# Optimization experiments

Hardware: AMD Instinct MI355X
Metric: run time of the kernel (lower is better)

The kernel has to match this reference:

```python
import jax, jax.numpy as jnp
import numpy as np

H, W = 512, 512
B, C = 16, 3
PCT = 3.0  # normalization_percentile_threshold


def _make_filter_map(h, w, d0_ratio=0.05, bn=1):
    d0 = int(max(d0_ratio * min(h, w) // 2, 1))  # = 12 for 512x512
    i = np.arange(h, dtype=np.float64)[:, None]
    j = np.arange(w, dtype=np.float64)[None, :]
    d = np.full((h, w), np.inf)
    for cx, cy in ((0, 0), (0, w - 1), (h - 1, w - 1), (h - 1, 0)):
        d = np.minimum(d, np.sqrt((i - cx) ** 2 + (j - cy) ** 2))
    fm = 1.0 / (1.0 + (d0 / (d + 1.0)) ** (2 * bn))
    # torch code assigns filter_map[j, i] -> transpose (no-op for square sizes)
    return jnp.asarray(fm.T.astype(np.float32))


def setup_inputs() -> dict:
    key = jax.random.key(0)
    k1, k2 = jax.random.split(key)
    x = jax.random.normal(k1, (B, C, H, W), dtype=jnp.float32)
    mask = (jax.random.uniform(k2, (B, C, H, W)) > 0.2).astype(jnp.float32)
    filter_map = _make_filter_map(H, W)
    return {"x": x, "mask": mask, "filter_map": filter_map}


def reference(x, mask, filter_map):
    b, c, h, w = x.shape
    n = h * w
    # median_padding: torch.median returns the lower middle element -> sorted index (n-1)//2
    med = jnp.sort(x.reshape(b, c, n), axis=-1)[..., (n - 1) // 2] + 0.2  # (B,C)
    xp = mask * x + (1.0 - mask) * med[:, :, None, None]
    # Butterworth high-pass in Fourier domain
    hfc = jnp.abs(jnp.fft.ifft2(jnp.fft.fft2(xp) * filter_map)).astype(jnp.float32)
    # per-(n,c) percentile normalization; .int() truncates toward zero -> jnp.trunc
    temp = jnp.trunc(hfc * 256.0) / 256.0
    lo = jnp.percentile(temp, PCT, axis=(-2, -1), keepdims=True)
    hi = jnp.percentile(temp, 100.0 - PCT, axis=(-2, -1), keepdims=True)
    res = (hfc - lo) / (hi - lo)
    return res * mask
```

## Files before the change

### kernel.cpp

```cpp
#include <hip/hip_runtime.h>
#include <math.h>


#define HN 512
#define WN 512
#define NPIX (HN * WN)
#define NCH 48
#define MED_K 131071u
#define TWOPI 6.283185307179586f

typedef unsigned int u32;
typedef float f4v __attribute__((ext_vector_type(4)));

__device__ __constant__ u32 PRANKS[4] = {7864u, 7865u, 254278u, 254279u};

__device__ __forceinline__ int rev8_9(int i) { return ((i & 7) << 6) | (i & 56) | (i >> 6); }

__device__ __forceinline__ int swz(int e) { return e ^ ((e >> 4) & 0xF); }

#define WB() __builtin_amdgcn_wave_barrier()

__device__ __forceinline__ u32 f2key(float f) {
  u32 u = __float_as_uint(f);
  return u ^ ((u & 0x80000000u) ? 0xFFFFFFFFu : 0x80000000u);
}
__device__ __forceinline__ float key2f(u32 k) {
  u32 u = (k & 0x80000000u) ? (k ^ 0x80000000u) : ~k;
  return __uint_as_float(u);
}

__device__ __forceinline__ float2 cadd(float2 a, float2 b) { return make_float2(a.x + b.x, a.y + b.y); }
__device__ __forceinline__ float2 csub(float2 a, float2 b) { return make_float2(a.x - b.x, a.y - b.y); }
__device__ __forceinline__ float2 cmul(float2 a, float2 b) {
  return make_float2(a.x * b.x - a.y * b.y, a.x * b.y + a.y * b.x);
}

template <bool INV>
__device__ __forceinline__ void dft8(float2* r) {
  const float S2 = 0.70710678118654752f;
  float2 e0, e1, e2, e3, o0, o1, o2, o3;
  {
    float2 t0 = cadd(r[0], r[4]), t1 = csub(r[0], r[4]);
    float2 t2 = cadd(r[2], r[6]), t3 = csub(r[2], r[6]);
    e0 = cadd(t0, t2); e2 = csub(t0, t2);
    if (!INV) { e1 = make_float2(t1.x + t3.y, t1.y - t3.x); e3 = make_float2(t1.x - t3.y, t1.y + t3.x); }
    else      { e1 = make_float2(t1.x - t3.y, t1.y + t3.x); e3 = make_float2(t1.x + t3.y, t1.y - t3.x); }
  }
  {
    float2 t0 = cadd(r[1], r[5]), t1 = csub(r[1], r[5]);
    float2 t2 = cadd(r[3], r[7]), t3 = csub(r[3], r[7]);
    o0 = cadd(t0, t2); o2 = csub(t0, t2);
    if (!INV) { o1 = make_float2(t1.x + t3.y, t1.y - t3.x); o3 = make_float2(t1.x - t3.y, t1.y + t3.x); }
    else      { o1 = make_float2(t1.x - t3.y, t1.y + t3.x); o3 = make_float2(t1.x + t3.y, t1.y - t3.x); }
  }
  float2 w1o, w2o, w3o;
  if (!INV) {
    w1o = make_float2(S2 * (o1.x + o1.y), S2 * (o1.y - o1.x));
    w2o = make_float2(o2.y, -o2.x);
    w3o = make_float2(S2 * (o3.y - o3.x), -S2 * (o3.x + o3.y));
  } else {
    w1o = make_float2(S2 * (o1.x - o1.y), S2 * (o1.x + o1.y));
    w2o = make_float2(-o2.y, o2.x);
    w3o = make_float2(-S2 * (o3.x + o3.y), S2 * (o3.x - o3.y));
  }
  r[0] = cadd(e0, o0); r[4] = csub(e0, o0);
  r[1] = cadd(e1, w1o); r[5] = csub(e1, w1o);
  r[2] = cadd(e2, w2o); r[6] = csub(e2, w2o);
  r[3] = cadd(e3, w3o); r[7] = csub(e3, w3o);
}

__device__ __forceinline__ void twid(float2* r, float ang) {
  float sn, cs;
  __sincosf(ang, &sn, &cs);
  float2 w = make_float2(cs, sn);
  float2 wj = w;
  r[1] = cmul(r[1], wj);
  #pragma unroll
  for (int j = 2; j < 8; ++j) { wj = cmul(wj, w); r[j] = cmul(r[j], wj); }
}

__device__ void scan_find(const u32* __restrict__ h, int per, u32 rank,
                          u32* out_bin, u32* out_pref) {
  __shared__ u32 csum[256], cpre[256];
  int t = threadIdx.x;
  u32 s = 0;
  for (int i = 0; i < per; ++i) s += h[t * per + i];
  csum[t] = s;
  __syncthreads();
  if (t == 0) { u32 a = 0; for (int i = 0; i < 256; ++i) { cpre[i] = a; a += csum[i]; } }
  __syncthreads();
  if (cpre[t] <= rank && rank < cpre[t] + csum[t]) {
    u32 acc = cpre[t];
    for (int i = 0; i < per; ++i) {
      u32 c = h[t * per + i];
      if (rank < acc + c) { *out_bin = (u32)(t * per + i); *out_pref = acc; break; }
      acc += c;
    }
  }
  __syncthreads();
}


__global__ __launch_bounds__(256) void kmed1(const float4* __restrict__ x4, u32* __restrict__ h1) {
  int ch = blockIdx.x >> 4, s = blockIdx.x & 15;
  __shared__ u32 lh[4096];
  for (int i = threadIdx.x; i < 4096; i += 256) lh[i] = 0;
  __syncthreads();
  const float4* p = x4 + (size_t)ch * (NPIX / 4) + (size_t)s * (NPIX / 64);
  for (int i = threadIdx.x; i < NPIX / 64; i += 256) {
    float4 v = p[i];
    atomicAdd(&lh[f2key(v.x) >> 20], 1u);
    atomicAdd(&lh[f2key(v.y) >> 20], 1u);
    atomicAdd(&lh[f2key(v.z) >> 20], 1u);
    atomicAdd(&lh[f2key(v.w) >> 20], 1u);
  }
  __syncthreads();
  u32* h = h1 + (size_t)ch * 4096;
  for (int i = threadIdx.x; i < 4096; i += 256) { u32 c = lh[i]; if (c) atomicAdd(&h[i], c); }
}

__global__ __launch_bounds__(256) void kscan1(const u32* __restrict__ h1, u32* sel1, u32* pref1) {
  __shared__ u32 b, p;
  scan_find(h1 + (size_t)blockIdx.x * 4096, 16, MED_K, &b, &p);
  if (threadIdx.x == 0) { sel1[blockIdx.x] = b; pref1[blockIdx.x] = p; }
}

__global__ __launch_bounds__(256) void kmed2(const float4* __restrict__ x4, u32* __restrict__ h2,
                                             const u32* __restrict__ sel1) {
  int ch = blockIdx.x >> 4, s = blockIdx.x & 15;
  u32 sh = sel1[ch];
  __shared__ u32 lh[4096];
  for (int i = threadIdx.x; i < 4096; i += 256) lh[i] = 0;
  __syncthreads();
  const float4* p = x4 + (size_t)ch * (NPIX / 4) + (size_t)s * (NPIX / 64);
  for (int i = threadIdx.x; i < NPIX / 64; i += 256) {
    float4 v = p[i];
    u32 k;
    k = f2key(v.x); if ((k >> 20) == sh) atomicAdd(&lh[(k >> 8) & 0xFFFu], 1u);
    k = f2key(v.y); if ((k >> 20) == sh) atomicAdd(&lh[(k >> 8) & 0xFFFu], 1u);
    k = f2key(v.z); if ((k >> 20) == sh) atomicAdd(&lh[(k >> 8) & 0xFFFu], 1u);
    k = f2key(v.w); if ((k >> 20) == sh) atomicAdd(&lh[(k >> 8) & 0xFFFu], 1u);
  }
  __syncthreads();
  u32* h = h2 + (size_t)ch * 4096;
  for (int i = threadIdx.x; i < 4096; i += 256) { u32 c = lh[i]; if (c) atomicAdd(&h[i], c); }
}

__global__ __launch_bounds__(256) void kscan2(const u32* __restrict__ h2, const u32* __restrict__ pref1,
                                              u32* sel2, u32* pref2) {
  __shared__ u32 b, p;
  scan_find(h2 + (size_t)blockIdx.x * 4096, 16, MED_K - pref1[blockIdx.x], &b, &p);
  if (threadIdx.x == 0) { sel2[blockIdx.x] = b; pref2[blockIdx.x] = p; }
}

__global__ __launch_bounds__(256) void kmed3(const float4* __restrict__ x4, u32* __restrict__ h3,
                                             const u32* __restrict__ sel1, const u32* __restrict__ sel2) {
  int ch = blockIdx.x >> 4, s = blockIdx.x & 15;
  u32 pre = (sel1[ch] << 12) | sel2[ch];
  __shared__ u32 lh[256];
  lh[threadIdx.x] = 0;
  __syncthreads();
  const float4* p = x4 + (size_t)ch * (NPIX / 4) + (size_t)s * (NPIX / 64);
  for (int i = threadIdx.x; i < NPIX / 64; i += 256) {
    float4 v = p[i];
    u32 k;
    k = f2key(v.x); if ((k >> 8) == pre) atomicAdd(&lh[k & 0xFFu], 1u);
    k = f2key(v.y); if ((k >> 8) == pre) atomicAdd(&lh[k & 0xFFu], 1u);
    k = f2key(v.z); if ((k >> 8) == pre) atomicAdd(&lh[k & 0xFFu], 1u);
    k = f2key(v.w); if ((k >> 8) == pre) atomicAdd(&lh[k & 0xFFu], 1u);
  }
  __syncthreads();
  u32 c = lh[threadIdx.x];
  if (c) atomicAdd(&h3[(size_t)ch * 256 + threadIdx.x], c);
}

__global__ __launch_bounds__(256) void kscan3(const u32* __restrict__ h3, const u32* __restrict__ sel1,
                                              const u32* __restrict__ sel2, const u32* __restrict__ pref1,
                                              const u32* __restrict__ pref2, float* med) {
  int ch = blockIdx.x;
  __shared__ u32 b, p;
  scan_find(h3 + (size_t)ch * 256, 1, MED_K - pref1[ch] - pref2[ch], &b, &p);
  if (threadIdx.x == 0) {
    u32 key = (sel1[ch] << 20) | (sel2[ch] << 8) | b;
    med[ch] = key2f(key) + 0.2f;
  }
}


__global__ __launch_bounds__(256) void kperm(const float* __restrict__ fmap, float* __restrict__ fmp) {
  int c = blockIdx.x;
  for (int e = threadIdx.x; e < HN; e += 256)
    fmp[(size_t)c * HN + e] = fmap[(size_t)rev8_9(e) * WN + rev8_9(c)] * (1.0f / (float)NPIX);
}


__global__ __launch_bounds__(256) void krow_fwd(const float* __restrict__ x, const float* __restrict__ mask,
                                                const float* __restrict__ med, float2* __restrict__ cbuf, int ch0) {
  int lch = blockIdx.x >> 7, rb = blockIdx.x & 127;
  int gch = ch0 + lch;
  int lane = threadIdx.x & 63, r = threadIdx.x >> 6;
  int row = rb * 4 + r;
  __shared__ float2 lds[4][512];
  float2* L = lds[r];
  float mv = med[gch];
  const float* xr = x + (size_t)gch * NPIX + (size_t)row * WN;
  const float* mr = mask + (size_t)gch * NPIX + (size_t)row * WN;
  float2 rg[8];
  #pragma unroll
  for (int m = 0; m < 8; ++m) {
    float xv = xr[lane + 64 * m], mm = mr[lane + 64 * m];
    rg[m] = make_float2(mm * xv + (1.0f - mm) * mv, 0.0f);
  }
  dft8<false>(rg);
  twid(rg, (float)lane * (-TWOPI / 512.0f));
  #pragma unroll
  for (int j = 0; j < 8; ++j) L[swz(lane + 64 * j)] = rg[j];
  WB();
  int eb = 64 * (lane >> 3) + (lane & 7);
  #pragma unroll
  for (int m = 0; m < 8; ++m) rg[m] = L[swz(eb + 8 * m)];
  dft8<false>(rg);
  twid(rg, (float)(lane & 7) * (-TWOPI / 64.0f));
  #pragma unroll
  for (int j = 0; j < 8; ++j) L[swz(eb + 8 * j)] = rg[j];
  WB();
  int pcb = (8 * lane) ^ ((lane >> 1) & 0xF);
  #pragma unroll
  for (int m = 0; m < 8; ++m) rg[m] = L[pcb ^ m];
  dft8<false>(rg);
  #pragma unroll
  for (int j = 0; j < 8; ++j) L[pcb ^ j] = rg[j];
  WB();
  float2* cb = cbuf + (size_t)lch * NPIX + (size_t)row * WN;
  #pragma unroll
  for (int q = 0; q < 4; ++q) {
    int e = 2 * (lane + 64 * q);
    int s = swz(e);
    float2 a = L[s], b = L[s ^ 1];
    *(float4*)(cb + e) = make_float4(a.x, a.y, b.x, b.y);
  }
}


__global__ __launch_bounds__(1024, 8) void kcol(float2* __restrict__ cbuf, const float* __restrict__ fmp) {
  int lch = blockIdx.x >> 5;
  int c0 = (blockIdx.x & 31) << 4;
  int tid = threadIdx.x;
  int lane = tid & 63, w = tid >> 6;
  __shared__ float2 lds[16][512];
  float2* L = lds[w];
  size_t base = (size_t)lch * NPIX + c0;
  #pragma unroll
  for (int it = 0; it < 4; ++it) {
    int g = it * 1024 + tid;
    int h = g >> 3, qq = g & 7;
    float4 v = *(const float4*)(cbuf + base + (size_t)h * WN + 2 * qq);
    int sh = swz(h);
    lds[2 * qq][sh]     = make_float2(v.x, v.y);
    lds[2 * qq + 1][sh] = make_float2(v.z, v.w);
  }
  __syncthreads();
  float2 rg[8];
  int eb = 64 * (lane >> 3) + (lane & 7);
  int pcb = (8 * lane) ^ ((lane >> 1) & 0xF);
  #pragma unroll
  for (int m = 0; m < 8; ++m) rg[m] = L[swz(lane + 64 * m)];
  dft8<false>(rg);
  twid(rg, (float)lane * (-TWOPI / 512.0f));
  #pragma unroll
  for (int j = 0; j < 8; ++j) L[swz(lane + 64 * j)] = rg[j];
  WB();
  #pragma unroll
  for (int m = 0; m < 8; ++m) rg[m] = L[swz(eb + 8 * m)];
  dft8<false>(rg);
  twid(rg, (float)(lane & 7) * (-TWOPI / 64.0f));
  #pragma unroll
  for (int j = 0; j < 8; ++j) L[swz(eb + 8 * j)] = rg[j];
  WB();
  #pragma unroll
  for (int m = 0; m < 8; ++m) rg[m] = L[pcb ^ m];
  dft8<false>(rg);
  {
    const float* fp = fmp + (size_t)(c0 + w) * HN + 8 * lane;
    float4 f0 = *(const float4*)fp, f1 = *(const float4*)(fp + 4);
    rg[0].x *= f0.x; rg[0].y *= f0.x;  rg[1].x *= f0.y; rg[1].y *= f0.y;
    rg[2].x *= f0.z; rg[2].y *= f0.z;  rg[3].x *= f0.w; rg[3].y *= f0.w;
    rg[4].x *= f1.x; rg[4].y *= f1.x;  rg[5].x *= f1.y; rg[5].y *= f1.y;
    rg[6].x *= f1.z; rg[6].y *= f1.z;  rg[7].x *= f1.w; rg[7].y *= f1.w;
  }
  dft8<true>(rg);
  #pragma unroll
  for (int j = 0; j < 8; ++j) L[pcb ^ j] = rg[j];
  WB();
  #pragma unroll
  for (int m = 0; m < 8; ++m) rg[m] = L[swz(eb + 8 * m)];
  twid(rg, (float)(lane & 7) * (TWOPI / 64.0f));
  dft8<true>(rg);
  #pragma unroll
  for (int j = 0; j < 8; ++j) L[swz(eb + 8 * j)] = rg[j];
  WB();
  #pragma unroll
  for (int m = 0; m < 8; ++m) rg[m] = L[swz(lane + 64 * m)];
  twid(rg, (float)lane * (TWOPI / 512.0f));
  dft8<true>(rg);
  #pragma unroll
  for (int j = 0; j < 8; ++j) L[swz(lane + 64 * j)] = rg[j];
  __syncthreads();
  #pragma unroll
  for (int it = 0; it < 4; ++it) {
    int g = it * 1024 + tid;
    int h = g >> 3, qq = g & 7;
    int sh = swz(h);
    float2 a = lds[2 * qq][sh], b = lds[2 * qq + 1][sh];
    *(float4*)(cbuf + base + (size_t)h * WN + 2 * qq) = make_float4(a.x, a.y, b.x, b.y);
  }
}


__global__ __launch_bounds__(256) void krow_inv(const float2* __restrict__ cbuf, float* __restrict__ out,
                                                u32* __restrict__ hc, int ch0) {
  int lch = blockIdx.x >> 7, rb = blockIdx.x & 127;
  int gch = ch0 + lch;
  int lane = threadIdx.x & 63, r = threadIdx.x >> 6;
  int row = rb * 4 + r;
  __shared__ float2 lds[4][512];
  __shared__ u32 lh[4][256];
  float2* L = lds[r];
  u32* H = lh[r];
  #pragma unroll
  for (int i = 0; i < 4; ++i) H[lane + 64 * i] = 0;
  const float2* cb = cbuf + (size_t)lch * NPIX + (size_t)row * WN;
  #pragma unroll
  for (int q = 0; q < 4; ++q) {
    int e = 2 * (lane + 64 * q);
    float4 v = *(const float4*)(cb + e);
    int s = swz(e);
    L[s]     = make_float2(v.x, v.y);
    L[s ^ 1] = make_float2(v.z, v.w);
  }
  WB();
  float2 rg[8];
  int pcb = (8 * lane) ^ ((lane >> 1) & 0xF);
  #pragma unroll
  for (int m = 0; m < 8; ++m) rg[m] = L[pcb ^ m];
  dft8<true>(rg);
  #pragma unroll
  for (int j = 0; j < 8; ++j) L[pcb ^ j] = rg[j];
  WB();
  int eb = 64 * (lane >> 3) + (lane & 7);
  #pragma unroll
  for (int m = 0; m < 8; ++m) rg[m] = L[swz(eb + 8 * m)];
  twid(rg, (float)(lane & 7) * (TWOPI / 64.0f));
  dft8<true>(rg);
  #pragma unroll
  for (int j = 0; j < 8; ++j) L[swz(eb + 8 * j)] = rg[j];
  WB();
  #pragma unroll
  for (int m = 0; m < 8; ++m) rg[m] = L[swz(lane + 64 * m)];
  twid(rg, (float)lane * (TWOPI / 512.0f));
  dft8<true>(rg);
  float* orow = out + (size_t)gch * NPIX + (size_t)row * WN;
  u32 binv[8];
  #pragma unroll
  for (int j = 0; j < 8; ++j) {
    float mg = sqrtf(rg[j].x * rg[j].x + rg[j].y * rg[j].y);
    orow[lane + 64 * j] = mg;
    binv[j] = ((u32)fminf(mg * 256.0f, 65535.0f)) >> 8;
  }
  #pragma unroll 1
  for (int j = 0; j < 8; ++j) {
    u32 bin = binv[j];
    unsigned long long todo = __ballot(1);
    while (todo) {
      int src = (int)(__ffsll((unsigned long long)todo) - 1);
      u32 b = (u32)__shfl((int)bin, src);
      unsigned long long mt = __ballot(bin == b);
      if (lane == src) atomicAdd(&H[b], (u32)__popcll(mt));
      todo &= ~mt;
    }
  }
  #pragma unroll
  for (int i = 0; i < 4; ++i) {
    u32 c = H[lane + 64 * i];
    if (c) atomicAdd(&hc[(size_t)gch * 256 + lane + 64 * i], c);
  }
}


__global__ __launch_bounds__(256) void kpcts1(const u32* __restrict__ hc, u32* selc, u32* prefc) {
  int ch = blockIdx.x;
  __shared__ u32 b, p;
  for (int q = 0; q < 4; ++q) {
    scan_find(hc + (size_t)ch * 256, 1, PRANKS[q], &b, &p);
    if (threadIdx.x == 0) { selc[ch * 4 + q] = b; prefc[ch * 4 + q] = p; }
    __syncthreads();
  }
}

__global__ __launch_bounds__(256) void kpctf(const float4* __restrict__ out4, u32* __restrict__ hf,
                                             const u32* __restrict__ selc) {
  int ch = blockIdx.x >> 3, s = blockIdx.x & 7;
  u32 t0 = selc[ch * 4 + 0], t1 = selc[ch * 4 + 1], t2 = selc[ch * 4 + 2], t3 = selc[ch * 4 + 3];
  __shared__ u32 lh[1024];
  for (int i = threadIdx.x; i < 1024; i += 256) lh[i] = 0;
  __syncthreads();
  const float4* p = out4 + (size_t)ch * (NPIX / 4) + (size_t)s * (NPIX / 32);
  for (int i = threadIdx.x; i < NPIX / 32; i += 256) {
    float4 v = p[i];
    float vv[4] = {v.x, v.y, v.z, v.w};
    #pragma unroll
    for (int j = 0; j < 4; ++j) {
      u32 bin = (u32)fminf(vv[j] * 256.0f, 65535.0f);
      u32 cb = bin >> 8, fb = bin & 255u;
      if (cb == t0) atomicAdd(&lh[0 * 256 + fb], 1u);
      if (cb == t1) atomicAdd(&lh[1 * 256 + fb], 1u);
      if (cb == t2) atomicAdd(&lh[2 * 256 + fb], 1u);
      if (cb == t3) atomicAdd(&lh[3 * 256 + fb], 1u);
    }
  }
  __syncthreads();
  for (int i = threadIdx.x; i < 1024; i += 256) {
    u32 c = lh[i];
    if (c) atomicAdd(&hf[(size_t)ch * 1024 + i], c);
  }
}

__global__ __launch_bounds__(256) void kpcts2(const u32* __restrict__ hf, const u32* __restrict__ selc,
                                              const u32* __restrict__ prefc, float* lov, float* invv) {
  int ch = blockIdx.x;
  __shared__ u32 b, p;
  __shared__ u32 bins[4];
  for (int q = 0; q < 4; ++q) {
    scan_find(hf + (size_t)ch * 1024 + q * 256, 1, PRANKS[q] - prefc[ch * 4 + q], &b, &p);
    if (threadIdx.x == 0) bins[q] = (selc[ch * 4 + q] << 8) | b;
    __syncthreads();
  }
  if (threadIdx.x == 0) {
    double vlo = 0.03 * (double)(NPIX - 1);
    double vhi = 0.97 * (double)(NPIX - 1);
    double glo = vlo - floor(vlo);
    double ghi = vhi - floor(vhi);
    double l0 = bins[0] / 256.0, l1 = bins[1] / 256.0;
    double h0 = bins[2] / 256.0, h1 = bins[3] / 256.0;
    double lo = l0 + glo * (l1 - l0);
    double hi = h0 + ghi * (h1 - h0);
    lov[ch] = (float)lo;
    invv[ch] = (float)(1.0 / (hi - lo));
  }
}


__global__ __launch_bounds__(256) void kfinal(float4* __restrict__ o4, const float4* __restrict__ m4,
                                              const float* __restrict__ lov, const float* __restrict__ invv) {
  size_t i = (size_t)blockIdx.x * 256 + threadIdx.x;
  int ch = (int)(i >> 16);
  float lo = lov[ch], iv = invv[ch];
  float4 o = o4[i], m = m4[i];
  f4v res;
  res.x = (o.x - lo) * iv * m.x;
  res.y = (o.y - lo) * iv * m.y;
  res.z = (o.z - lo) * iv * m.z;
  res.w = (o.w - lo) * iv * m.w;
  __builtin_nontemporal_store(res, (f4v*)&o4[i]);
}


extern "C" void kernel_launch(void* const* d_in, const int* in_sizes, int n_in,
                              void* d_out, int out_size, void* d_ws, size_t ws_size,
                              hipStream_t stream) {
  (void)in_sizes; (void)n_in; (void)out_size;
  const float* x = (const float*)d_in[0];
  const float* mask = (const float*)d_in[1];
  const float* fmap = (const float*)d_in[2];
  float* out = (float*)d_out;
  char* ws = (char*)d_ws;

  size_t off = 0;
  u32* h1 = (u32*)(ws + off); off += (size_t)NCH * 4096 * 4;
  u32* h2 = (u32*)(ws + off); off += (size_t)NCH * 4096 * 4;
  u32* h3 = (u32*)(ws + off); off += (size_t)NCH * 256 * 4;
  u32* hc = (u32*)(ws + off); off += (size_t)NCH * 256 * 4;
  u32* hf = (u32*)(ws + off); off += (size_t)NCH * 1024 * 4;
  const size_t HIST_BYTES = off;
  u32* sel1  = (u32*)(ws + off); off += NCH * 4;
  u32* pref1 = (u32*)(ws + off); off += NCH * 4;
  u32* sel2  = (u32*)(ws + off); off += NCH * 4;
  u32* pref2 = (u32*)(ws + off); off += NCH * 4;
  u32* selc  = (u32*)(ws + off); off += NCH * 16;
  u32* prefc = (u32*)(ws + off); off += NCH * 16;
  float* med  = (float*)(ws + off); off += NCH * 4;
  float* lov  = (float*)(ws + off); off += NCH * 4;
  float* invv = (float*)(ws + off); off += NCH * 4;
  off = (off + 4095) & ~(size_t)4095;
  float* fmp = (float*)(ws + off); off += (size_t)NPIX * 4;
  off = (off + 255) & ~(size_t)255;
  float2* cbuf = (float2*)(ws + off);

  size_t avail = (ws_size > off) ? ws_size - off : 0;
  int cpc = 1;
  const int cands[8] = {48, 24, 16, 12, 8, 4, 2, 1};
  for (int i = 0; i < 8; ++i) {
    if ((size_t)cands[i] * NPIX * sizeof(float2) <= avail) { cpc = cands[i]; break; }
  }

  (void)hipMemsetAsync(ws, 0, HIST_BYTES, stream);
  kperm<<<WN, 256, 0, stream>>>(fmap, fmp);

  kmed1<<<NCH * 16, 256, 0, stream>>>((const float4*)x, h1);
  kscan1<<<NCH, 256, 0, stream>>>(h1, sel1, pref1);
  kmed2<<<NCH * 16, 256, 0, stream>>>((const float4*)x, h2, sel1);
  kscan2<<<NCH, 256, 0, stream>>>(h2, pref1, sel2, pref2);
  kmed3<<<NCH * 16, 256, 0, stream>>>((const float4*)x, h3, sel1, sel2);
  kscan3<<<NCH, 256, 0, stream>>>(h3, sel1, sel2, pref1, pref2, med);

  for (int ch0 = 0; ch0 < NCH; ch0 += cpc) {
    int cc = (NCH - ch0 < cpc) ? (NCH - ch0) : cpc;
    krow_fwd<<<cc * 128, 256, 0, stream>>>(x, mask, med, cbuf, ch0);
    kcol<<<cc * 32, 1024, 0, stream>>>(cbuf, fmp);
    krow_inv<<<cc * 128, 256, 0, stream>>>(cbuf, out, hc, ch0);
  }

  kpcts1<<<NCH, 256, 0, stream>>>(hc, selc, prefc);
  kpctf<<<NCH * 8, 256, 0, stream>>>((const float4*)out, hf, selc);
  kpcts2<<<NCH, 256, 0, stream>>>(hf, selc, prefc, lov, invv);

  kfinal<<<(NCH * NPIX / 4) / 256, 256, 0, stream>>>((float4*)out, (const float4*)mask, lov, invv);
}
```

Measured before the change: 366.8 us.

## Compact median candidates and build percentile histogram inside inverse row FFT

The three-pass radix median is replaced by one histogram pass plus a pass that compacts the keys falling in the median's top-level bin into a candidate list. A single block per channel then resolves the remaining bits from that list, avoiding a third full read of x. The percentile stage now builds a 4096-bin histogram (1/256 resolution) directly in krow_inv, which removes the coarse/fine two-pass histogram that reread the whole output. It also splits kmed1's shared histogram in two to reduce atomic contention and caps the FFT channel chunk at 16. The costs are heavier shared-memory atomics and LDS use in krow_inv, and a fixed candidate capacity that would break correctness if more than 32768 keys land in the median's bin.

Measured after the change: 379.9 us. +3.6%, slower.

```diff
diff --git a/kernel.cpp b/kernel.cpp
--- a/kernel.cpp
+++ b/kernel.cpp
@@ -8,6 +8,7 @@
 #define NCH 48
 #define MED_K 131071u
 #define TWOPI 6.283185307179586f
+#define CAP 32768
 
 typedef unsigned int u32;
 typedef float f4v __attribute__((ext_vector_type(4)));
@@ -103,85 +104,89 @@
 
 __global__ __launch_bounds__(256) void kmed1(const float4* __restrict__ x4, u32* __restrict__ h1) {
   int ch = blockIdx.x >> 4, s = blockIdx.x & 15;
-  __shared__ u32 lh[4096];
-  for (int i = threadIdx.x; i < 4096; i += 256) lh[i] = 0;
-  __syncthreads();
+  __shared__ u32 lh[8193];
+  for (int i = threadIdx.x; i < 8193; i += 256) lh[i] = 0;
+  __syncthreads();
+  int co = (threadIdx.x & 1) * 4097;
   const float4* p = x4 + (size_t)ch * (NPIX / 4) + (size_t)s * (NPIX / 64);
   for (int i = threadIdx.x; i < NPIX / 64; i += 256) {
     float4 v = p[i];
-    atomicAdd(&lh[f2key(v.x) >> 20], 1u);
-    atomicAdd(&lh[f2key(v.y) >> 20], 1u);
-    atomicAdd(&lh[f2key(v.z) >> 20], 1u);
-    atomicAdd(&lh[f2key(v.w) >> 20], 1u);
+    atomicAdd(&lh[(f2key(v.x) >> 20) + co], 1u);
+    atomicAdd(&lh[(f2key(v.y) >> 20) + co], 1u);
+    atomicAdd(&lh[(f2key(v.z) >> 20) + co], 1u);
+    atomicAdd(&lh[(f2key(v.w) >> 20) + co], 1u);
   }
   __syncthreads();
   u32* h = h1 + (size_t)ch * 4096;
-  for (int i = threadIdx.x; i < 4096; i += 256) { u32 c = lh[i]; if (c) atomicAdd(&h[i], c); }
-}
-
-__global__ __launch_bounds__(256) void kscan1(const u32* __restrict__ h1, u32* sel1, u32* pref1) {
-  __shared__ u32 b, p;
-  scan_find(h1 + (size_t)blockIdx.x * 4096, 16, MED_K, &b, &p);
-  if (threadIdx.x == 0) { sel1[blockIdx.x] = b; pref1[blockIdx.x] = p; }
-}
-
-__global__ __launch_bounds__(256) void kmed2(const float4* __restrict__ x4, u32* __restrict__ h2,
-                                             const u32* __restrict__ sel1) {
+  for (int i = threadIdx.x; i < 4096; i += 256) {
+    u32 c = lh[i] + lh[i + 4097];
+    if (c) atomicAdd(&h[i], c);
+  }
+}
+
+
+__global__ __launch_bounds__(256) void kmed2(const float4* __restrict__ x4, const u32* __restrict__ h1,
+                                             u32* __restrict__ cnt, u32* __restrict__ cand) {
   int ch = blockIdx.x >> 4, s = blockIdx.x & 15;
-  u32 sh = sel1[ch];
-  __shared__ u32 lh[4096];
-  for (int i = threadIdx.x; i < 4096; i += 256) lh[i] = 0;
-  __syncthreads();
+  __shared__ u32 sb, sp;
+  scan_find(h1 + (size_t)ch * 4096, 16, MED_K, &sb, &sp);
+  u32 sel1 = sb;
   const float4* p = x4 + (size_t)ch * (NPIX / 4) + (size_t)s * (NPIX / 64);
+  u32* cl = cand + (size_t)ch * CAP;
+  int lane = threadIdx.x & 63;
   for (int i = threadIdx.x; i < NPIX / 64; i += 256) {
     float4 v = p[i];
-    u32 k;
-    k = f2key(v.x); if ((k >> 20) == sh) atomicAdd(&lh[(k >> 8) & 0xFFFu], 1u);
-    k = f2key(v.y); if ((k >> 20) == sh) atomicAdd(&lh[(k >> 8) & 0xFFFu], 1u);
-    k = f2key(v.z); if ((k >> 20) == sh) atomicAdd(&lh[(k >> 8) & 0xFFFu], 1u);
-    k = f2key(v.w); if ((k >> 20) == sh) atomicAdd(&lh[(k >> 8) & 0xFFFu], 1u);
-  }
-  __syncthreads();
-  u32* h = h2 + (size_t)ch * 4096;
-  for (int i = threadIdx.x; i < 4096; i += 256) { u32 c = lh[i]; if (c) atomicAdd(&h[i], c); }
-}
-
-__global__ __launch_bounds__(256) void kscan2(const u32* __restrict__ h2, const u32* __restrict__ pref1,
-                                              u32* sel2, u32* pref2) {
-  __shared__ u32 b, p;
-  scan_find(h2 + (size_t)blockIdx.x * 4096, 16, MED_K - pref1[blockIdx.x], &b, &p);
-  if (threadIdx.x == 0) { sel2[blockIdx.x] = b; pref2[blockIdx.x] = p; }
-}
-
-__global__ __launch_bounds__(256) void kmed3(const float4* __restrict__ x4, u32* __restrict__ h3,
-                                             const u32* __restrict__ sel1, const u32* __restrict__ sel2) {
-  int ch = blockIdx.x >> 4, s = blockIdx.x & 15;
-  u32 pre = (sel1[ch] << 12) | sel2[ch];
-  __shared__ u32 lh[256];
+    u32 ks[4] = {f2key(v.x), f2key(v.y), f2key(v.z), f2key(v.w)};
+    #pragma unroll
+    for (int j = 0; j < 4; ++j) {
+      bool m = (ks[j] >> 20) == sel1;
+      unsigned long long mk = __ballot(m);
+      if (mk) {
+        int src = (int)(__ffsll(mk) - 1);
+        u32 base = 0;
+        if (lane == src) base = atomicAdd(&cnt[ch], (u32)__popcll(mk));
+        base = (u32)__shfl((int)base, src);
+        if (m) {
+          u32 off = (u32)__popcll(mk & ((1ull << lane) - 1ull));
+          u32 idx = base + off;
+          if (idx < CAP) cl[idx] = ks[j] & 0xFFFFFu;
+        }
+      }
+    }
+  }
+}
+
+
+__global__ __launch_bounds__(256) void kmedfin(const u32* __restrict__ h1, const u32* __restrict__ cand,
+                                               float* __restrict__ med) {
+  int ch = blockIdx.x;
+  __shared__ u32 sb, sp;
+  __shared__ u32 lh[4096];
+  scan_find(h1 + (size_t)ch * 4096, 16, MED_K, &sb, &sp);
+  u32 sel1 = sb;
+  u32 rank2 = MED_K - sp;
+  u32 n = h1[(size_t)ch * 4096 + sel1];
+  if (n > CAP) n = CAP;
+  for (int i = threadIdx.x; i < 4096; i += 256) lh[i] = 0;
+  __syncthreads();
+  const u32* cl = cand + (size_t)ch * CAP;
+  for (int i = threadIdx.x; i < (int)n; i += 256) atomicAdd(&lh[(cl[i] >> 8) & 0xFFFu], 1u);
+  __syncthreads();
+  scan_find(lh, 16, rank2, &sb, &sp);
+  u32 sel2 = sb;
+  u32 rank3 = rank2 - sp;
+  __syncthreads();
   lh[threadIdx.x] = 0;
   __syncthreads();
-  const float4* p = x4 + (size_t)ch * (NPIX / 4) + (size_t)s * (NPIX / 64);
-  for (int i = threadIdx.x; i < NPIX / 64; i += 256) {
-    float4 v = p[i];
-    u32 k;
-    k = f2key(v.x); if ((k >> 8) == pre) atomicAdd(&lh[k & 0xFFu], 1u);
-    k = f2key(v.y); if ((k >> 8) == pre) atomicAdd(&lh[k & 0xFFu], 1u);
-    k = f2key(v.z); if ((k >> 8) == pre) atomicAdd(&lh[k & 0xFFu], 1u);
-    k = f2key(v.w); if ((k >> 8) == pre) atomicAdd(&lh[k & 0xFFu], 1u);
-  }
-  __syncthreads();
-  u32 c = lh[threadIdx.x];
-  if (c) atomicAdd(&h3[(size_t)ch * 256 + threadIdx.x], c);
-}
-
-__global__ __launch_bounds__(256) void kscan3(const u32* __restrict__ h3, const u32* __restrict__ sel1,
-                                              const u32* __restrict__ sel2, const u32* __restrict__ pref1,
-                                              const u32* __restrict__ pref2, float* med) {
-  int ch = blockIdx.x;
-  __shared__ u32 b, p;
-  scan_find(h3 + (size_t)ch * 256, 1, MED_K - pref1[ch] - pref2[ch], &b, &p);
+  for (int i = threadIdx.x; i < (int)n; i += 256) {
+    u32 c = cl[i];
+    if (((c >> 8) & 0xFFFu) == sel2) atomicAdd(&lh[c & 0xFFu], 1u);
+  }
+  __syncthreads();
   if (threadIdx.x == 0) {
-    u32 key = (sel1[ch] << 20) | (sel2[ch] << 8) | b;
+    u32 acc = 0, b = 0;
+    for (int i = 0; i < 256; ++i) { u32 c = lh[i]; if (rank3 < acc + c) { b = (u32)i; break; } acc += c; }
+    u32 key = (sel1 << 20) | (sel2 << 8) | b;
     med[ch] = key2f(key) + 0.2f;
   }
 }
@@ -318,17 +323,16 @@
 
 
 __global__ __launch_bounds__(256) void krow_inv(const float2* __restrict__ cbuf, float* __restrict__ out,
-                                                u32* __restrict__ hc, int ch0) {
+                                                u32* __restrict__ hfine, int ch0) {
   int lch = blockIdx.x >> 7, rb = blockIdx.x & 127;
   int gch = ch0 + lch;
   int lane = threadIdx.x & 63, r = threadIdx.x >> 6;
   int row = rb * 4 + r;
   __shared__ float2 lds[4][512];
-  __shared__ u32 lh[4][256];
+  __shared__ u32 fh[4096];
   float2* L = lds[r];
-  u32* H = lh[r];
-  #pragma unroll
-  for (int i = 0; i < 4; ++i) H[lane + 64 * i] = 0;
+  for (int i = threadIdx.x; i < 4096; i += 256) fh[i] = 0;
+  __syncthreads();
   const float2* cb = cbuf + (size_t)lch * NPIX + (size_t)row * WN;
   #pragma unroll
   for (int q = 0; q < 4; ++q) {
@@ -360,79 +364,30 @@
   twid(rg, (float)lane * (TWOPI / 512.0f));
   dft8<true>(rg);
   float* orow = out + (size_t)gch * NPIX + (size_t)row * WN;
-  u32 binv[8];
   #pragma unroll
   for (int j = 0; j < 8; ++j) {
     float mg = sqrtf(rg[j].x * rg[j].x + rg[j].y * rg[j].y);
     orow[lane + 64 * j] = mg;
-    binv[j] = ((u32)fminf(mg * 256.0f, 65535.0f)) >> 8;
-  }
-  #pragma unroll 1
-  for (int j = 0; j < 8; ++j) {
-    u32 bin = binv[j];
-    unsigned long long todo = __ballot(1);
-    while (todo) {
-      int src = (int)(__ffsll((unsigned long long)todo) - 1);
-      u32 b = (u32)__shfl((int)bin, src);
-      unsigned long long mt = __ballot(bin == b);
-      if (lane == src) atomicAdd(&H[b], (u32)__popcll(mt));
-      todo &= ~mt;
-    }
-  }
-  #pragma unroll
-  for (int i = 0; i < 4; ++i) {
-    u32 c = H[lane + 64 * i];
-    if (c) atomicAdd(&hc[(size_t)gch * 256 + lane + 64 * i], c);
-  }
-}
-
-
-__global__ __launch_bounds__(256) void kpcts1(const u32* __restrict__ hc, u32* selc, u32* prefc) {
+    u32 bin = (u32)fminf(mg * 256.0f, 4095.0f);
+    atomicAdd(&fh[bin], 1u);
+  }
+  __syncthreads();
+  for (int i = threadIdx.x; i < 4096; i += 256) {
+    u32 c = fh[i];
+    if (c) atomicAdd(&hfine[(size_t)gch * 4096 + i], c);
+  }
+}
+
+
+__global__ __launch_bounds__(256) void kpct(const u32* __restrict__ hfine,
+                                            float* __restrict__ lov, float* __restrict__ invv) {
   int ch = blockIdx.x;
-  __shared__ u32 b, p;
+  __shared__ u32 sb, sp;
+  __shared__ u32 bins[4];
+  const u32* h = hfine + (size_t)ch * 4096;
   for (int q = 0; q < 4; ++q) {
-    scan_find(hc + (size_t)ch * 256, 1, PRANKS[q], &b, &p);
-    if (threadIdx.x == 0) { selc[ch * 4 + q] = b; prefc[ch * 4 + q] = p; }
-    __syncthreads();
-  }
-}
-
-__global__ __launch_bounds__(256) void kpctf(const float4* __restrict__ out4, u32* __restrict__ hf,
-                                             const u32* __restrict__ selc) {
-  int ch = blockIdx.x >> 3, s = blockIdx.x & 7;
-  u32 t0 = selc[ch * 4 + 0], t1 = selc[ch * 4 + 1], t2 = selc[ch * 4 + 2], t3 = selc[ch * 4 + 3];
-  __shared__ u32 lh[1024];
-  for (int i = threadIdx.x; i < 1024; i += 256) lh[i] = 0;
-  __syncthreads();
-  const float4* p = out4 + (size_t)ch * (NPIX / 4) + (size_t)s * (NPIX / 32);
-  for (int i = threadIdx.x; i < NPIX / 32; i += 256) {
-    float4 v = p[i];
-    float vv[4] = {v.x, v.y, v.z, v.w};
-    #pragma unroll
-    for (int j = 0; j < 4; ++j) {
-      u32 bin = (u32)fminf(vv[j] * 256.0f, 65535.0f);
-      u32 cb = bin >> 8, fb = bin & 255u;
-      if (cb == t0) atomicAdd(&lh[0 * 256 + fb], 1u);
-      if (cb == t1) atomicAdd(&lh[1 * 256 + fb], 1u);
-      if (cb == t2) atomicAdd(&lh[2 * 256 + fb], 1u);
-      if (cb == t3) atomicAdd(&lh[3 * 256 + fb], 1u);
-    }
-  }
-  __syncthreads();
-  for (int i = threadIdx.x; i < 1024; i += 256) {
-    u32 c = lh[i];
-    if (c) atomicAdd(&hf[(size_t)ch * 1024 + i], c);
-  }
-}
-
-__global__ __launch_bounds__(256) void kpcts2(const u32* __restrict__ hf, const u32* __restrict__ selc,
-                                              const u32* __restrict__ prefc, float* lov, float* invv) {
-  int ch = blockIdx.x;
-  __shared__ u32 b, p;
-  __shared__ u32 bins[4];
-  for (int q = 0; q < 4; ++q) {
-    scan_find(hf + (size_t)ch * 1024 + q * 256, 1, PRANKS[q] - prefc[ch * 4 + q], &b, &p);
-    if (threadIdx.x == 0) bins[q] = (selc[ch * 4 + q] << 8) | b;
+    scan_find(h, 16, PRANKS[q], &sb, &sp);
+    if (threadIdx.x == 0) bins[q] = sb;
     __syncthreads();
   }
   if (threadIdx.x == 0) {
@@ -476,53 +431,40 @@
   char* ws = (char*)d_ws;
 
   size_t off = 0;
-  u32* h1 = (u32*)(ws + off); off += (size_t)NCH * 4096 * 4;
-  u32* h2 = (u32*)(ws + off); off += (size_t)NCH * 4096 * 4;
-  u32* h3 = (u32*)(ws + off); off += (size_t)NCH * 256 * 4;
-  u32* hc = (u32*)(ws + off); off += (size_t)NCH * 256 * 4;
-  u32* hf = (u32*)(ws + off); off += (size_t)NCH * 1024 * 4;
-  const size_t HIST_BYTES = off;
-  u32* sel1  = (u32*)(ws + off); off += NCH * 4;
-  u32* pref1 = (u32*)(ws + off); off += NCH * 4;
-  u32* sel2  = (u32*)(ws + off); off += NCH * 4;
-  u32* pref2 = (u32*)(ws + off); off += NCH * 4;
-  u32* selc  = (u32*)(ws + off); off += NCH * 16;
-  u32* prefc = (u32*)(ws + off); off += NCH * 16;
+  u32* h1    = (u32*)(ws + off); off += (size_t)NCH * 4096 * 4;
+  u32* hfine = (u32*)(ws + off); off += (size_t)NCH * 4096 * 4;
+  u32* cnt   = (u32*)(ws + off); off += (size_t)NCH * 4;
+  const size_t ZBYTES = off;
   float* med  = (float*)(ws + off); off += NCH * 4;
   float* lov  = (float*)(ws + off); off += NCH * 4;
   float* invv = (float*)(ws + off); off += NCH * 4;
-  off = (off + 4095) & ~(size_t)4095;
+  off = (off + 255) & ~(size_t)255;
+  u32* cand = (u32*)(ws + off); off += (size_t)NCH * CAP * 4;
   float* fmp = (float*)(ws + off); off += (size_t)NPIX * 4;
   off = (off + 255) & ~(size_t)255;
   float2* cbuf = (float2*)(ws + off);
 
   size_t avail = (ws_size > off) ? ws_size - off : 0;
   int cpc = 1;
-  const int cands[8] = {48, 24, 16, 12, 8, 4, 2, 1};
-  for (int i = 0; i < 8; ++i) {
+  const int cands[6] = {16, 12, 8, 4, 2, 1};
+  for (int i = 0; i < 6; ++i) {
     if ((size_t)cands[i] * NPIX * sizeof(float2) <= avail) { cpc = cands[i]; break; }
   }
 
-  (void)hipMemsetAsync(ws, 0, HIST_BYTES, stream);
+  (void)hipMemsetAsync(ws, 0, ZBYTES, stream);
   kperm<<<WN, 256, 0, stream>>>(fmap, fmp);
 
   kmed1<<<NCH * 16, 256, 0, stream>>>((const float4*)x, h1);
-  kscan1<<<NCH, 256, 0, stream>>>(h1, sel1, pref1);
-  kmed2<<<NCH * 16, 256, 0, stream>>>((const float4*)x, h2, sel1);
-  kscan2<<<NCH, 256, 0, stream>>>(h2, pref1, sel2, pref2);
-  kmed3<<<NCH * 16, 256, 0, stream>>>((const float4*)x, h3, sel1, sel2);
-  kscan3<<<NCH, 256, 0, stream>>>(h3, sel1, sel2, pref1, pref2, med);
+  kmed2<<<NCH * 16, 256, 0, stream>>>((const float4*)x, h1, cnt, cand);
+  kmedfin<<<NCH, 256, 0, stream>>>(h1, cand, med);
 
   for (int ch0 = 0; ch0 < NCH; ch0 += cpc) {
     int cc = (NCH - ch0 < cpc) ? (NCH - ch0) : cpc;
     krow_fwd<<<cc * 128, 256, 0, stream>>>(x, mask, med, cbuf, ch0);
     kcol<<<cc * 32, 1024, 0, stream>>>(cbuf, fmp);
-    krow_inv<<<cc * 128, 256, 0, stream>>>(cbuf, out, hc, ch0);
-  }
-
-  kpcts1<<<NCH, 256, 0, stream>>>(hc, selc, prefc);
-  kpctf<<<NCH * 8, 256, 0, stream>>>((const float4*)out, hf, selc);
-  kpcts2<<<NCH, 256, 0, stream>>>(hf, selc, prefc, lov, invv);
-
+    krow_inv<<<cc * 128, 256, 0, stream>>>(cbuf, out, hfine, ch0);
+  }
+
+  kpct<<<NCH, 256, 0, stream>>>(hfine, lov, invv);
   kfinal<<<(NCH * NPIX / 4) / 256, 256, 0, stream>>>((float4*)out, (const float4*)mask, lov, invv);
 }
```
